# Kernel tuning notes

Hardware: AMD Instinct MI355X
Metric: run time of the kernel (lower is better)

The kernel has to match this reference:

```python
import math
import jax, jax.numpy as jnp
import numpy as np

LOG_K = 9          # log_kernel_size
SIGMA_MIN = 0.5
SIGMA_MAX = 10.0


def setup_inputs() -> dict:
    key = jax.random.key(0)
    k1, k2 = jax.random.split(key)
    B, C, H, W = 4, 3, 256, 256
    x = jax.random.normal(k1, (B, C, H, W), dtype=jnp.float32)
    # foa_xy holds (x, y) pixel coordinates of the focus of attention
    foa_xy = jax.random.uniform(k2, (B, 2), dtype=jnp.float32) * jnp.array([W - 1, H - 1], jnp.float32)
    return {"x": x, "foa_xy": foa_xy}


def _log_per_pixel_kernels(foa_xy, H, W, k, sigma_min, sigma_max):
    """Per-pixel LoG kernels, shape [B, k*k, H*W] (out_ch=in_ch=1 spatial-only)."""
    B = foa_xy.shape[0]
    kk = k * k
    # pixel coordinate grid (x, y), flattened row-major: [HW, 2]
    yy, xx = jnp.meshgrid(jnp.arange(H), jnp.arange(W), indexing="ij")
    xx_yy = jnp.stack([xx.ravel(), yy.ravel()], axis=-1).astype(jnp.float32)
    # squared distances within the kernel window: [kk]
    r = jnp.arange(-(k // 2), k // 2 + 1)
    ryy, rxx = jnp.meshgrid(r, r, indexing="ij")
    r_sq = (rxx ** 2 + ryy ** 2).reshape(-1).astype(jnp.float32)
    # distance of every pixel from the FOA: [B, HW]
    diff = xx_yy[None, :, :] - foa_xy[:, None, :]
    dists = jnp.sqrt(jnp.sum(diff ** 2, axis=-1))
    diag = math.sqrt(H * H + W * W)
    dn = dists / diag
    sigma = (1.0 - dn) * sigma_min + dn * sigma_max        # linear sigma, [B, HW]
    s = sigma[:, None, :]                                   # [B, 1, HW]
    tmp = r_sq[None, :, None] / (2.0 * s * s)               # [B, kk, HW]
    factor = -1.0 / (math.pi * s ** 4)
    kern = factor * (1.0 - tmp) * jnp.exp(-tmp)
    kern = kern * jnp.sqrt(s)                               # scale_factor = sigma**0.5
    kern = kern * dists[:, None, :]                         # distance modulation
    return kern                                             # [B, kk, HW]


def reference(x, foa_xy):
    B, C, H, W = x.shape
    k = LOG_K
    pad = ((k - 1) * 1 + 1) // 2                            # dilation=1 -> 4
    xp = jnp.pad(x, ((0, 0), (0, 0), (pad, pad), (pad, pad)), mode="reflect")
    # im2col: [B, C*kk, H, W], feature dim ordered (channel-major, then kernel pos)
    patches = jax.lax.conv_general_dilated_patches(xp, (k, k), (1, 1), "VALID")
    patches = patches.reshape(B, C, k * k, H * W)
    kern = _log_per_pixel_kernels(foa_xy, H, W, k, SIGMA_MIN, SIGMA_MAX)  # [B, kk, HW]
    # spatial-only kernel: sum over kernel-area dim, broadcast over channels
    out = jnp.einsum("bckp,bkp->bcp", patches, kern)
    return out.reshape(B, C, H, W)
```

## Files before the change

kernel.cpp:

```cpp
#include <hip/hip_runtime.h>
#include <math.h>

#define HH 256
#define WW 256
#define CC 3
#define HW (HH*WW)

#define TW 64
#define TH 8
#define IW 72
#define IH 16
#define LDS_CH (IW*IH)
#define LDS_TOT (LDS_CH*CC)

__device__ __forceinline__ int reflect(int v, int n) {
    v = (v < 0) ? -v : v;
    v = (v > n - 1) ? (2 * (n - 1) - v) : v;
    return v;
}

__device__ __forceinline__ constexpr int r2idx(int r2) {
    switch (r2) {
        case 0:  return 0;  case 1:  return 1;  case 2:  return 2;  case 4:  return 3;
        case 5:  return 4;  case 8:  return 5;  case 9:  return 6;  case 10: return 7;
        case 13: return 8;  case 16: return 9;  case 17: return 10; case 18: return 11;
        case 20: return 12; case 25: return 13; case 26: return 14; default: return 15;
    }
}

__global__ __launch_bounds__(256) void adaptive_log_kernel(
    const float* __restrict__ x, const float* __restrict__ foa,
    float* __restrict__ out)
{
    __shared__ float lds[LDS_TOT];
    const int tid = threadIdx.x;
    const int bx = blockIdx.x & 3;
    const int by = blockIdx.x >> 2;
    const int b  = blockIdx.y;

    const int gx0 = bx * TW;
    const int gy0 = by * TH;

    const float* xb = x + (size_t)b * (CC * HW);
    for (int i = tid; i < LDS_TOT; i += 256) {
        int c   = i / LDS_CH;
        int rem = i - c * LDS_CH;
        int r   = rem / IW;
        int col = rem - r * IW;
        int gr = reflect(gy0 + r - 4, HH);
        int gc = reflect(gx0 + col - 4, WW);
        lds[i] = xb[c * HW + gr * WW + gc];
    }
    __syncthreads();

    const int tx = tid & 31;
    const int ty = tid >> 5;

    const int px0 = gx0 + tx * 2;
    const int py  = gy0 + ty;

    const float fx = foa[2 * b + 0];
    const float fy = foa[2 * b + 1];

    float w0[16], w1[16];
    #pragma unroll
    for (int o = 0; o < 2; ++o) {
        float* w = o ? w1 : w0;
        const float ddx = (float)(px0 + o) - fx;
        const float ddy = (float)py - fy;
        const float dist = sqrtf(ddx * ddx + ddy * ddy);
        const float dn = dist * (1.0f / 362.03867196751236f);
        const float sigma = 0.5f + 9.5f * dn;
        const float s2 = sigma * sigma;
        const float inv2s2 = 0.5f / s2;
        const float common = (-1.0f / (float)M_PI) / (s2 * s2) * sqrtf(sigma) * dist;
        const float q  = __expf(-inv2s2);
        const float q2 = q * q;
        const float q4 = q2 * q2;
        const float q8 = q4 * q4;
        const float q16 = q8 * q8;
        float e[16];
        e[0] = 1.0f;      e[1] = q;          e[2] = q2;         e[3] = q4;
        e[4] = q4 * q;    e[5] = q8;         e[6] = q8 * q;     e[7] = q8 * q2;
        e[8] = q8 * q4 * q;            e[9] = q16;        e[10] = q16 * q;
        e[11] = q16 * q2; e[12] = q16 * q4;  e[13] = q16 * q8 * q;
        e[14] = q16 * q8 * q2;         e[15] = q16 * q16;
        const float r2v[16] = {0,1,2,4,5,8,9,10,13,16,17,18,20,25,26,32};
        #pragma unroll
        for (int k = 0; k < 16; ++k)
            w[k] = common * (1.0f - r2v[k] * inv2s2) * e[k];
    }

    float acc0[CC] = {0.f, 0.f, 0.f};
    float acc1[CC] = {0.f, 0.f, 0.f};
    #pragma unroll
    for (int c = 0; c < CC; ++c) {
        #pragma unroll
        for (int i = 0; i < 9; ++i) {
            const float2* row = (const float2*)&lds[c * LDS_CH + (ty + i) * IW + tx * 2];
            const float2 f01 = row[0];
            const float2 f23 = row[1];
            const float2 f45 = row[2];
            const float2 f67 = row[3];
            const float2 f89 = row[4];
            const float f[10] = {f01.x, f01.y, f23.x, f23.y, f45.x,
                                 f45.y, f67.x, f67.y, f89.x, f89.y};
            const int dy2 = (i - 4) * (i - 4);
            float s0 = 0.f, s1 = 0.f;
            #pragma unroll
            for (int m = 0; m < 9; ++m) {
                const int dx2 = (m - 4) * (m - 4);
                s0 += w0[r2idx(dy2 + dx2)] * f[m];
                s1 += w1[r2idx(dy2 + dx2)] * f[m + 1];
            }
            acc0[c] += s0;
            acc1[c] += s1;
        }
    }

    float* ob = out + (size_t)b * (CC * HW) + py * WW + px0;
    #pragma unroll
    for (int c = 0; c < CC; ++c) {
        *(float2*)&ob[c * HW] = make_float2(acc0[c], acc1[c]);
    }
}

extern "C" void kernel_launch(void* const* d_in, const int* in_sizes, int n_in,
                              void* d_out, int out_size, void* d_ws, size_t ws_size,
                              hipStream_t stream) {
    const float* x   = (const float*)d_in[0];
    const float* foa = (const float*)d_in[1];
    float* out = (float*)d_out;

    dim3 grid(4 * 32, 4);
    dim3 block(256);
    adaptive_log_kernel<<<grid, block, 0, stream>>>(x, foa, out);
}
```

Baseline: 65.24 us.

## Drop LDS tiling and read input rows directly from global memory per output row

Replaces the shared-memory tile staging with direct global float2 loads, so each 128-thread block computes one full image row and fetches its nine reflected input rows through the cache hierarchy. Reflection is handled with precomputed row offsets and a slow path for edge columns only. This removes the LDS fill loop and the barrier, and adds more blocks. The cost is redundant global/L2 traffic, since each input row is now read by nine blocks, and float2 loads at x0-4 may be misaligned. The weight formula is also algebraically refactored to save a multiply per weight.

```diff
diff --git a/kernel.cpp b/kernel.cpp
--- a/kernel.cpp
+++ b/kernel.cpp
@@ -5,13 +5,6 @@
 #define WW 256
 #define CC 3
 #define HW (HH*WW)
-
-#define TW 64
-#define TH 8
-#define IW 72
-#define IH 16
-#define LDS_CH (IW*IH)
-#define LDS_TOT (LDS_CH*CC)
 
 __device__ __forceinline__ int reflect(int v, int n) {
     v = (v < 0) ? -v : v;
@@ -28,101 +21,97 @@
     }
 }
 
-__global__ __launch_bounds__(256) void adaptive_log_kernel(
+__global__ __launch_bounds__(128) void adaptive_log_kernel(
     const float* __restrict__ x, const float* __restrict__ foa,
     float* __restrict__ out)
 {
-    __shared__ float lds[LDS_TOT];
     const int tid = threadIdx.x;
-    const int bx = blockIdx.x & 3;
-    const int by = blockIdx.x >> 2;
-    const int b  = blockIdx.y;
+    const int y   = blockIdx.x;
+    const int b   = blockIdx.y;
+    const int x0  = tid * 2;
 
-    const int gx0 = bx * TW;
-    const int gy0 = by * TH;
-
-    const float* xb = x + (size_t)b * (CC * HW);
-    for (int i = tid; i < LDS_TOT; i += 256) {
-        int c   = i / LDS_CH;
-        int rem = i - c * LDS_CH;
-        int r   = rem / IW;
-        int col = rem - r * IW;
-        int gr = reflect(gy0 + r - 4, HH);
-        int gc = reflect(gx0 + col - 4, WW);
-        lds[i] = xb[c * HW + gr * WW + gc];
-    }
-    __syncthreads();
-
-    const int tx = tid & 31;
-    const int ty = tid >> 5;
-
-    const int px0 = gx0 + tx * 2;
-    const int py  = gy0 + ty;
+    int ryo[9];
+    #pragma unroll
+    for (int i = 0; i < 9; ++i)
+        ryo[i] = reflect(y + i - 4, HH) * WW;
 
     const float fx = foa[2 * b + 0];
     const float fy = foa[2 * b + 1];
 
-    float w0[16], w1[16];
+    float w[2][16];
     #pragma unroll
     for (int o = 0; o < 2; ++o) {
-        float* w = o ? w1 : w0;
-        const float ddx = (float)(px0 + o) - fx;
-        const float ddy = (float)py - fy;
+        const float ddx = (float)(x0 + o) - fx;
+        const float ddy = (float)y - fy;
         const float dist = sqrtf(ddx * ddx + ddy * ddy);
         const float dn = dist * (1.0f / 362.03867196751236f);
         const float sigma = 0.5f + 9.5f * dn;
         const float s2 = sigma * sigma;
         const float inv2s2 = 0.5f / s2;
         const float common = (-1.0f / (float)M_PI) / (s2 * s2) * sqrtf(sigma) * dist;
-        const float q  = __expf(-inv2s2);
-        const float q2 = q * q;
-        const float q4 = q2 * q2;
-        const float q8 = q4 * q4;
+        const float q   = __expf(-inv2s2);
+        const float q2  = q * q;
+        const float q4  = q2 * q2;
+        const float q5  = q4 * q;
+        const float q8  = q4 * q4;
         const float q16 = q8 * q8;
-        float e[16];
-        e[0] = 1.0f;      e[1] = q;          e[2] = q2;         e[3] = q4;
-        e[4] = q4 * q;    e[5] = q8;         e[6] = q8 * q;     e[7] = q8 * q2;
-        e[8] = q8 * q4 * q;            e[9] = q16;        e[10] = q16 * q;
-        e[11] = q16 * q2; e[12] = q16 * q4;  e[13] = q16 * q8 * q;
-        e[14] = q16 * q8 * q2;         e[15] = q16 * q16;
+        const float e0 = 1.0f,  e1 = q,        e2 = q2,       e4 = q4;
+        const float e5 = q5,    e8 = q8,       e9 = q8 * q,   e10 = q8 * q2;
+        const float e13 = q8 * q5,  e16 = q16, e17 = q16 * q, e18 = q16 * q2;
+        const float e20 = q16 * q4, e25 = q16 * q8 * q, e26 = q16 * q8 * q2;
+        const float e32 = q16 * q16;
+        const float ee[16]  = {e0,e1,e2,e4,e5,e8,e9,e10,e13,e16,e17,e18,e20,e25,e26,e32};
         const float r2v[16] = {0,1,2,4,5,8,9,10,13,16,17,18,20,25,26,32};
+        const float cb = common * inv2s2;
         #pragma unroll
         for (int k = 0; k < 16; ++k)
-            w[k] = common * (1.0f - r2v[k] * inv2s2) * e[k];
+            w[o][k] = (common - r2v[k] * cb) * ee[k];
     }
+
+    const float* xb = x + (size_t)b * (CC * HW);
+    const bool edge = (x0 < 4) || (x0 > 250);
 
     float acc0[CC] = {0.f, 0.f, 0.f};
     float acc1[CC] = {0.f, 0.f, 0.f};
+
     #pragma unroll
     for (int c = 0; c < CC; ++c) {
+        const float* xc = xb + c * HW;
         #pragma unroll
         for (int i = 0; i < 9; ++i) {
-            const float2* row = (const float2*)&lds[c * LDS_CH + (ty + i) * IW + tx * 2];
-            const float2 f01 = row[0];
-            const float2 f23 = row[1];
-            const float2 f45 = row[2];
-            const float2 f67 = row[3];
-            const float2 f89 = row[4];
-            const float f[10] = {f01.x, f01.y, f23.x, f23.y, f45.x,
-                                 f45.y, f67.x, f67.y, f89.x, f89.y};
+            const float* rowp = xc + ryo[i];
+            float f[10];
+            if (!edge) {
+                const float2* rp = (const float2*)(rowp + (x0 - 4));
+                const float2 a0 = rp[0];
+                const float2 a1 = rp[1];
+                const float2 a2 = rp[2];
+                const float2 a3 = rp[3];
+                const float2 a4 = rp[4];
+                f[0]=a0.x; f[1]=a0.y; f[2]=a1.x; f[3]=a1.y; f[4]=a2.x;
+                f[5]=a2.y; f[6]=a3.x; f[7]=a3.y; f[8]=a4.x; f[9]=a4.y;
+            } else {
+                #pragma unroll
+                for (int j = 0; j < 10; ++j)
+                    f[j] = rowp[reflect(x0 - 4 + j, WW)];
+            }
             const int dy2 = (i - 4) * (i - 4);
             float s0 = 0.f, s1 = 0.f;
             #pragma unroll
             for (int m = 0; m < 9; ++m) {
                 const int dx2 = (m - 4) * (m - 4);
-                s0 += w0[r2idx(dy2 + dx2)] * f[m];
-                s1 += w1[r2idx(dy2 + dx2)] * f[m + 1];
+                s0 += w[0][r2idx(dy2 + dx2)] * f[m];
+                s1 += w[1][r2idx(dy2 + dx2)] * f[m + 1];
             }
             acc0[c] += s0;
             acc1[c] += s1;
         }
     }
 
-    float* ob = out + (size_t)b * (CC * HW) + py * WW + px0;
+    float* ob = out + (size_t)b * (CC * HW) + y * WW + x0;
     #pragma unroll
-    for (int c = 0; c < CC; ++c) {
+    for (int c = 0; c < CC; ++c)
         *(float2*)&ob[c * HW] = make_float2(acc0[c], acc1[c]);
-    }
 }
 
 extern "C" void kernel_launch(void* const* d_in, const int* in_sizes, int n_in,
@@ -132,7 +121,7 @@
     const float* foa = (const float*)d_in[1];
     float* out = (float*)d_out;
 
-    dim3 grid(4 * 32, 4);
-    dim3 block(256);
+    dim3 grid(HH, 4);
+    dim3 block(128);
     adaptive_log_kernel<<<grid, block, 0, stream>>>(x, foa, out);
 }
```

Result: slower. 85.59 us (+31.2%).
